# Kernel tuning notes

Hardware: AMD Instinct MI355X
Metric: run time of the kernel (lower is better)

## Reference

```python
import jax, jax.numpy as jnp
import numpy as np

END_TOKEN = 2


def setup_inputs() -> dict:
    key = jax.random.key(0)
    k1, k2, k3 = jax.random.split(key, 3)
    B, E, V, L = 256, 8, 32000, 128
    cur_proba = jax.random.normal(k1, (B * E, 1, V), dtype=jnp.float32)
    proba = jax.random.normal(k2, (B, E), dtype=jnp.float32)
    outs = jax.random.randint(k3, (L, B, E), 0, V, dtype=jnp.int64)
    is_ended = jnp.zeros((B, E), dtype=bool)
    return {"cur_proba": cur_proba, "proba": proba, "outs": outs, "is_ended": is_ended}


def reference(cur_proba, proba, outs, is_ended):
    # beam_add step of GreedyDecoder
    B, E = proba.shape
    L = outs.shape[0]
    V = cur_proba.shape[-1]
    cp = cur_proba.reshape(B, E, V)
    # ended beams: all logits -> -inf except end_token column -> 0
    cp = jnp.where(is_ended[:, :, None], -jnp.inf, cp)
    cp = cp.at[:, :, END_TOKEN].set(jnp.where(is_ended, 0.0, cp[:, :, END_TOKEN]))
    total = (proba[:, :, None] + cp).reshape(B, E * V)  # [B, E*V]
    top_p, idx = jax.lax.top_k(total, E)                # [B, E] each
    topk_voc = idx % V
    topk_beam = idx // V
    # reorder history and ended flags by selected parent beam
    outs_g = jnp.take_along_axis(
        outs, jnp.broadcast_to(topk_beam[None], (L, B, E)), axis=-1)
    ended_g = jnp.take_along_axis(is_ended, topk_beam, axis=-1)
    outs_new = jnp.concatenate([outs_g, topk_voc[None]], axis=0)  # [L+1, B, E]
    ended_new = jnp.logical_or(ended_g, topk_voc == END_TOKEN)
    cur_input = topk_voc.reshape(B * E, 1)
    return (cur_input, top_p, outs_new, ended_new, topk_beam)
```

## Files before the change

kernel.cpp:

```cpp
#include <hip/hip_runtime.h>

#define Bn 256
#define En 8
#define Vn 32000
#define Ln 128
#define BEn (Bn * En)
#define END_TOK 2
#define NV4 (Vn / 4)

#define OFF_CUR   0
#define OFF_TOPP  (BEn)
#define OFF_OUTS  (2 * BEn)
#define OFF_ENDED (2 * BEn + (Ln + 1) * BEn)
#define OFF_BEAM  (3 * BEn + (Ln + 1) * BEn)

#define NEG_INF (-__builtin_inff())
#define IDX_SENTINEL 0x7fffffff

#define THRESH 3.0f
#define CAP    512

__device__ __forceinline__ void wave_argmax(float& v, int& ix, int& ln) {
#pragma unroll
    for (int off = 32; off > 0; off >>= 1) {
        float v2 = __shfl_xor(v, off, 64);
        int   i2 = __shfl_xor(ix, off, 64);
        int   l2 = __shfl_xor(ln, off, 64);
        bool take = (v2 > v) || (v2 == v && i2 < ix);
        v  = take ? v2 : v;
        ix = take ? i2 : ix;
        ln = take ? l2 : ln;
    }
}

__global__ __launch_bounds__(256) void k_seg_topk(
        const float* __restrict__ cp, const float* __restrict__ proba,
        const int* __restrict__ ended,
        float* __restrict__ cand_v, int* __restrict__ cand_i) {
    const int be = blockIdx.x;
    const int e  = be & (En - 1);
    const int tid = threadIdx.x;
    const float pr = proba[be];

    __shared__ int   s_cnt;
    __shared__ float s_cv[CAP];
    __shared__ int   s_ci[CAP];
    __shared__ float sv[32];
    __shared__ int   si[32];

    if (ended[be] != 0) {
        if (tid == 0) {
            cand_v[be * 8 + 0] = pr + 0.0f;
            cand_i[be * 8 + 0] = e * Vn + END_TOK;
            const int vs[7] = {0, 1, 3, 4, 5, 6, 7};
            for (int k = 0; k < 7; ++k) {
                cand_v[be * 8 + 1 + k] = NEG_INF;
                cand_i[be * 8 + 1 + k] = e * Vn + vs[k];
            }
        }
        return;
    }

    if (tid == 0) s_cnt = 0;
    __syncthreads();

    const float4* row = (const float4*)(cp + (size_t)be * Vn);

    auto check4 = [&](float4 f, int v0) {
        float m = fmaxf(fmaxf(f.x, f.y), fmaxf(f.z, f.w));
        if (m > THRESH) {
            if (f.x > THRESH) { int p = atomicAdd(&s_cnt, 1); if (p < CAP) { s_cv[p] = f.x; s_ci[p] = v0;     } }
            if (f.y > THRESH) { int p = atomicAdd(&s_cnt, 1); if (p < CAP) { s_cv[p] = f.y; s_ci[p] = v0 + 1; } }
            if (f.z > THRESH) { int p = atomicAdd(&s_cnt, 1); if (p < CAP) { s_cv[p] = f.z; s_ci[p] = v0 + 2; } }
            if (f.w > THRESH) { int p = atomicAdd(&s_cnt, 1); if (p < CAP) { s_cv[p] = f.w; s_ci[p] = v0 + 3; } }
        }
    };

    int i = tid;
    for (int k = 0; k < 7; ++k, i += 1024) {
        float4 f0 = row[i];
        float4 f1 = row[i + 256];
        float4 f2 = row[i + 512];
        float4 f3 = row[i + 768];
        check4(f0, i * 4);
        check4(f1, (i + 256) * 4);
        check4(f2, (i + 512) * 4);
        check4(f3, (i + 768) * 4);
    }
    {
        float4 f0 = row[i];
        float4 f1 = row[i + 256];
        float4 f2 = row[i + 512];
        check4(f0, i * 4);
        check4(f1, (i + 256) * 4);
        check4(f2, (i + 512) * 4);
        if (i + 768 < NV4) {
            float4 f3 = row[i + 768];
            check4(f3, (i + 768) * 4);
        }
    }
    __syncthreads();
    const int cnt = s_cnt;
    const int lane = tid & 63;
    const int wid  = tid >> 6;

    if (cnt >= 8 && cnt <= CAP) {
        float bv0 = (tid       < cnt) ? pr + s_cv[tid]       : NEG_INF;
        int   bi0 = (tid       < cnt) ? s_ci[tid]            : IDX_SENTINEL;
        float bv1 = (tid + 256 < cnt) ? pr + s_cv[tid + 256] : NEG_INF;
        int   bi1 = (tid + 256 < cnt) ? s_ci[tid + 256]      : IDX_SENTINEL;

#pragma unroll
        for (int r = 0; r < 8; ++r) {
            bool s0 = (bv0 > bv1) || (bv0 == bv1 && bi0 < bi1);
            float lv = s0 ? bv0 : bv1;
            int   li = s0 ? bi0 : bi1;
            int   ll = lane;
            wave_argmax(lv, li, ll);
            if (ll == lane) {
                if (bi0 == li && bv0 == lv) { bv0 = NEG_INF; bi0 = IDX_SENTINEL; }
                else if (bi1 == li && bv1 == lv) { bv1 = NEG_INF; bi1 = IDX_SENTINEL; }
            }
            if (lane == r) { sv[wid * 8 + r] = lv; si[wid * 8 + r] = li; }
        }
        __syncthreads();
        if (wid == 0) {
            float cv2 = (lane < 32) ? sv[lane] : NEG_INF;
            int   ci2 = (lane < 32) ? si[lane] : IDX_SENTINEL;
#pragma unroll
            for (int r = 0; r < 8; ++r) {
                float lv = cv2; int li = ci2; int ll = lane;
                wave_argmax(lv, li, ll);
                if (ll == lane) { cv2 = NEG_INF; ci2 = IDX_SENTINEL; }
                if (lane == r) {
                    cand_v[be * 8 + r] = lv;
                    cand_i[be * 8 + r] = e * Vn + li;
                }
            }
        }
        return;
    }

    float bv[8];
    int   bi[8];
#pragma unroll
    for (int k = 0; k < 8; ++k) { bv[k] = NEG_INF; bi[k] = IDX_SENTINEL; }
    float mn = NEG_INF;
    int   mi = IDX_SENTINEL;

    auto proc = [&](float val, int v) {
        if (val > mn) {
            bool done = false;
#pragma unroll
            for (int k = 0; k < 8; ++k) {
                bool m = !done && (bv[k] == mn) && (bi[k] == mi);
                if (m) { bv[k] = val; bi[k] = v; }
                done = done || m;
            }
            mn = bv[0]; mi = bi[0];
#pragma unroll
            for (int k = 1; k < 8; ++k) {
                bool t = (bv[k] < mn) || (bv[k] == mn && bi[k] > mi);
                mn = t ? bv[k] : mn;
                mi = t ? bi[k] : mi;
            }
        }
    };

    for (int j = tid; j < NV4; j += 256) {
        float4 f = row[j];
        int v0 = j * 4;
        proc(pr + f.x, v0);
        proc(pr + f.y, v0 + 1);
        proc(pr + f.z, v0 + 2);
        proc(pr + f.w, v0 + 3);
    }

#pragma unroll
    for (int r = 0; r < 8; ++r) {
        float lv = bv[0]; int li = bi[0];
#pragma unroll
        for (int k = 1; k < 8; ++k) {
            bool t = (bv[k] > lv) || (bv[k] == lv && bi[k] < li);
            lv = t ? bv[k] : lv;
            li = t ? bi[k] : li;
        }
        int ll = lane;
        wave_argmax(lv, li, ll);
        if (ll == lane) {
            bool done = false;
#pragma unroll
            for (int k = 0; k < 8; ++k) {
                bool m = !done && (bi[k] == li) && (bv[k] == lv);
                if (m) { bv[k] = NEG_INF; bi[k] = IDX_SENTINEL; }
                done = done || m;
            }
        }
        if (lane == r) { sv[wid * 8 + r] = lv; si[wid * 8 + r] = li; }
    }
    __syncthreads();

    if (wid == 0) {
        float cv2 = (lane < 32) ? sv[lane] : NEG_INF;
        int   ci2 = (lane < 32) ? si[lane] : IDX_SENTINEL;
#pragma unroll
        for (int r = 0; r < 8; ++r) {
            float lv = cv2; int li = ci2; int ll = lane;
            wave_argmax(lv, li, ll);
            if (ll == lane) { cv2 = NEG_INF; ci2 = IDX_SENTINEL; }
            if (lane == r) {
                cand_v[be * 8 + r] = lv;
                cand_i[be * 8 + r] = e * Vn + li;
            }
        }
    }
}

__global__ __launch_bounds__(256) void k_merge_gather(
        const float* __restrict__ cand_v, const int* __restrict__ cand_i,
        const int* __restrict__ ended, const int* __restrict__ outs,
        float* __restrict__ dout) {
    const int b = blockIdx.x;
    const int tid = threadIdx.x;
    __shared__ int s_voc[8];
    __shared__ int s_beam[8];

    if (tid < 64) {
        const int lane = tid;
        float cv = cand_v[b * 64 + lane];
        int   ci = cand_i[b * 64 + lane];
#pragma unroll
        for (int r = 0; r < 8; ++r) {
            float lv = cv; int li = ci; int ll = lane;
            wave_argmax(lv, li, ll);
            if (ll == lane) { cv = NEG_INF; ci = IDX_SENTINEL; }
            if (lane == r) {
                unsigned u = (unsigned)li;
                int voc  = (int)(u % Vn);
                int beam = (int)(u / Vn);
                s_voc[r]  = voc;
                s_beam[r] = beam;
                dout[OFF_CUR  + b * 8 + r] = (float)voc;
                dout[OFF_TOPP + b * 8 + r] = lv;
                int endg = ended[b * 8 + beam];
                dout[OFF_ENDED + b * 8 + r] = (endg != 0 || voc == END_TOK) ? 1.0f : 0.0f;
                dout[OFF_BEAM  + b * 8 + r] = (float)beam;
            }
        }
    }
    __syncthreads();

    const int e    = tid & 7;
    const int l0   = tid >> 3;
    const int bm   = s_beam[e];
    const int base = b * 8;
    int g0 = outs[(l0      ) * BEn + base + bm];
    int g1 = outs[(l0 +  32) * BEn + base + bm];
    int g2 = outs[(l0 +  64) * BEn + base + bm];
    int g3 = outs[(l0 +  96) * BEn + base + bm];
    dout[OFF_OUTS + (l0      ) * BEn + base + e] = (float)g0;
    dout[OFF_OUTS + (l0 +  32) * BEn + base + e] = (float)g1;
    dout[OFF_OUTS + (l0 +  64) * BEn + base + e] = (float)g2;
    dout[OFF_OUTS + (l0 +  96) * BEn + base + e] = (float)g3;
    if (tid < 8) dout[OFF_OUTS + Ln * BEn + base + tid] = (float)s_voc[tid];
}

extern "C" void kernel_launch(void* const* d_in, const int* in_sizes, int n_in,
                              void* d_out, int out_size, void* d_ws, size_t ws_size,
                              hipStream_t stream) {
    const float* cp    = (const float*)d_in[0];
    const float* proba = (const float*)d_in[1];
    const int*   outs  = (const int*)d_in[2];
    const int*   ended = (const int*)d_in[3];
    float* dout = (float*)d_out;

    float* cand_v = (float*)d_ws;
    int*   cand_i = (int*)((char*)d_ws + BEn * 8 * sizeof(float));

    k_seg_topk<<<BEn, 256, 0, stream>>>(cp, proba, ended, cand_v, cand_i);
    k_merge_gather<<<Bn, 256, 0, stream>>>(cand_v, cand_i, ended, outs, dout);
}
```

Measured before the change: 68.17 us.

## Stream logit row through LDS with async global_load_lds and a 4-deep pipeline

Replaces the direct float4 register loads in the threshold-scan pass with per-wave asynchronous global-to-LDS loads (global_load_lds, 16 bytes per lane). Each wave keeps four chunks in flight and uses explicit vmcnt waits and scheduling barriers to overlap memory latency with the threshold checks. It also halves the candidate capacity to 256 so the first-stage selection keeps one candidate per thread. The risk is that the smaller cap sends more rows to the slow full-scan fallback, and the hand-written waitcnt logic is fragile.

Measured after the change: 69.72 us. 1.02x slower.

```diff
diff --git a/kernel.cpp b/kernel.cpp
--- a/kernel.cpp
+++ b/kernel.cpp
@@ -1,4 +1,5 @@
 #include <hip/hip_runtime.h>
+#include <stdint.h>
 
 #define Bn 256
 #define En 8
@@ -7,6 +8,7 @@
 #define BEn (Bn * En)
 #define END_TOK 2
 #define NV4 (Vn / 4)
+#define NCHUNK 125
 
 #define OFF_CUR   0
 #define OFF_TOPP  (BEn)
@@ -18,7 +20,7 @@
 #define IDX_SENTINEL 0x7fffffff
 
 #define THRESH 3.0f
-#define CAP    512
+#define CAP    256
 
 __device__ __forceinline__ void wave_argmax(float& v, int& ix, int& ln) {
 #pragma unroll
@@ -37,20 +39,23 @@
         const float* __restrict__ cp, const float* __restrict__ proba,
         const int* __restrict__ ended,
         float* __restrict__ cand_v, int* __restrict__ cand_i) {
-    const int be = blockIdx.x;
-    const int e  = be & (En - 1);
-    const int tid = threadIdx.x;
-    const float pr = proba[be];
-
-    __shared__ int   s_cnt;
-    __shared__ float s_cv[CAP];
-    __shared__ int   s_ci[CAP];
-    __shared__ float sv[32];
-    __shared__ int   si[32];
+    const int be   = blockIdx.x;
+    const int e    = be & (En - 1);
+    const int tid  = threadIdx.x;
+    const int w    = tid >> 6;
+    const int lane = tid & 63;
+
+    __shared__ float4 s_stage[4][4][64];
+    __shared__ int    s_cnt;
+    __shared__ float  s_cv[CAP];
+    __shared__ int    s_ci[CAP];
+    __shared__ float  sv[32];
+    __shared__ int    si[32];
 
     if (ended[be] != 0) {
         if (tid == 0) {
-            cand_v[be * 8 + 0] = pr + 0.0f;
+            float pr0 = proba[be];
+            cand_v[be * 8 + 0] = pr0 + 0.0f;
             cand_i[be * 8 + 0] = e * Vn + END_TOK;
             const int vs[7] = {0, 1, 3, 4, 5, 6, 7};
             for (int k = 0; k < 7; ++k) {
@@ -64,7 +69,7 @@
     if (tid == 0) s_cnt = 0;
     __syncthreads();
 
-    const float4* row = (const float4*)(cp + (size_t)be * Vn);
+    const float* rowf = cp + (size_t)be * Vn;
 
     auto check4 = [&](float4 f, int v0) {
         float m = fmaxf(fmaxf(f.x, f.y), fmaxf(f.z, f.w));
@@ -76,51 +81,54 @@
         }
     };
 
-    int i = tid;
-    for (int k = 0; k < 7; ++k, i += 1024) {
-        float4 f0 = row[i];
-        float4 f1 = row[i + 256];
-        float4 f2 = row[i + 512];
-        float4 f3 = row[i + 768];
-        check4(f0, i * 4);
-        check4(f1, (i + 256) * 4);
-        check4(f2, (i + 512) * 4);
-        check4(f3, (i + 768) * 4);
-    }
-    {
-        float4 f0 = row[i];
-        float4 f1 = row[i + 256];
-        float4 f2 = row[i + 512];
-        check4(f0, i * 4);
-        check4(f1, (i + 256) * 4);
-        check4(f2, (i + 512) * 4);
-        if (i + 768 < NV4) {
-            float4 f3 = row[i + 768];
-            check4(f3, (i + 768) * 4);
-        }
-    }
+    const int nch = (NCHUNK - w + 3) >> 2;
+
+    auto issue = [&](int j) {
+        int c = w + 4 * j;
+        const float* g = rowf + (size_t)c * 256 + lane * 4;
+        __builtin_amdgcn_global_load_lds((const uint32_t*)g,
+                                         (uint32_t*)&s_stage[w][j & 3][0],
+                                         16, 0, 0);
+    };
+    auto consume = [&](int j) {
+        float4 f = s_stage[w][j & 3][lane];
+        int strip = (w + 4 * j) * 64 + lane;
+        check4(f, strip * 4);
+    };
+
+    issue(0); issue(1); issue(2); issue(3);
+    int j = 0;
+    for (; j + 3 < nch; ++j) {
+        asm volatile("s_waitcnt vmcnt(3)" ::: "memory");
+        __builtin_amdgcn_sched_barrier(0);
+        consume(j);
+        __builtin_amdgcn_sched_barrier(0);
+        if (j + 4 < nch) issue(j + 4);
+    }
+    asm volatile("s_waitcnt vmcnt(2)" ::: "memory");
+    __builtin_amdgcn_sched_barrier(0);
+    consume(j++);
+    asm volatile("s_waitcnt vmcnt(1)" ::: "memory");
+    __builtin_amdgcn_sched_barrier(0);
+    consume(j++);
+    asm volatile("s_waitcnt vmcnt(0)" ::: "memory");
+    __builtin_amdgcn_sched_barrier(0);
+    consume(j);
+
     __syncthreads();
     const int cnt = s_cnt;
-    const int lane = tid & 63;
-    const int wid  = tid >> 6;
+    const float pr = proba[be];
+    const int wid = w;
 
     if (cnt >= 8 && cnt <= CAP) {
-        float bv0 = (tid       < cnt) ? pr + s_cv[tid]       : NEG_INF;
-        int   bi0 = (tid       < cnt) ? s_ci[tid]            : IDX_SENTINEL;
-        float bv1 = (tid + 256 < cnt) ? pr + s_cv[tid + 256] : NEG_INF;
-        int   bi1 = (tid + 256 < cnt) ? s_ci[tid + 256]      : IDX_SENTINEL;
+        float bv0 = (tid < cnt) ? pr + s_cv[tid] : NEG_INF;
+        int   bi0 = (tid < cnt) ? s_ci[tid]      : IDX_SENTINEL;
 
 #pragma unroll
         for (int r = 0; r < 8; ++r) {
-            bool s0 = (bv0 > bv1) || (bv0 == bv1 && bi0 < bi1);
-            float lv = s0 ? bv0 : bv1;
-            int   li = s0 ? bi0 : bi1;
-            int   ll = lane;
+            float lv = bv0; int li = bi0; int ll = lane;
             wave_argmax(lv, li, ll);
-            if (ll == lane) {
-                if (bi0 == li && bv0 == lv) { bv0 = NEG_INF; bi0 = IDX_SENTINEL; }
-                else if (bi1 == li && bv1 == lv) { bv1 = NEG_INF; bi1 = IDX_SENTINEL; }
-            }
+            if (ll == lane && bi0 == li && bv0 == lv) { bv0 = NEG_INF; bi0 = IDX_SENTINEL; }
             if (lane == r) { sv[wid * 8 + r] = lv; si[wid * 8 + r] = li; }
         }
         __syncthreads();
@@ -167,9 +175,10 @@
         }
     };
 
-    for (int j = tid; j < NV4; j += 256) {
-        float4 f = row[j];
-        int v0 = j * 4;
+    const float4* row4 = (const float4*)rowf;
+    for (int q = tid; q < NV4; q += 256) {
+        float4 f = row4[q];
+        int v0 = q * 4;
         proc(pr + f.x, v0);
         proc(pr + f.y, v0 + 1);
         proc(pr + f.z, v0 + 2);
```
